# Kernel tuning notes

Hardware: AMD Instinct MI355X
Metric: run time of the kernel (lower is better)

Reference implementation:

```python
import jax, jax.numpy as jnp
import numpy as np

DIM = 1024
NUM_HEADS = 16
DIM_PER_HEAD = 64
INNER = NUM_HEADS * DIM_PER_HEAD  # 1024
SCALE = DIM_PER_HEAD ** -0.5
EPS = 1e-10


def setup_inputs() -> dict:
    key = jax.random.key(0)
    k_x, k_m, k_qkv, k_wo, k_bo = jax.random.split(key, 5)
    b, l = 2, 2048
    x = jax.random.normal(k_x, (b, l, DIM), dtype=jnp.float32)
    # binary multiplicative mask [b, l, l]
    mask = jax.random.randint(k_m, (b, l, l), 0, 2).astype(jnp.float32)
    # nn.Linear(dim, 3*inner, bias=False): weight [3*inner, dim]; we store transposed [dim, 3*inner]
    W_qkv = jax.random.normal(k_qkv, (DIM, 3 * INNER), dtype=jnp.float32) * (DIM ** -0.5)
    W_out = jax.random.normal(k_wo, (INNER, DIM), dtype=jnp.float32) * (INNER ** -0.5)
    b_out = jax.random.normal(k_bo, (DIM,), dtype=jnp.float32) * 0.01
    return {"x": x, "mask": mask, "W_qkv": W_qkv, "W_out": W_out, "b_out": b_out}


def reference(x, mask, W_qkv, W_out, b_out):
    b, l, d = x.shape
    qkv = x @ W_qkv  # [b, l, 3*inner]
    qkv = qkv.reshape(b, l, 3, NUM_HEADS, DIM_PER_HEAD)
    qkv = jnp.transpose(qkv, (2, 0, 3, 1, 4))  # [3, b, h, l, dh]
    q, k, v = qkv[0], qkv[1], qkv[2]
    # softmax FIRST (no additive mask), matching the original module
    attn = jax.nn.softmax(jnp.einsum('bhid,bhjd->bhij', q, k) * SCALE, axis=-1)  # [b,h,l,l]
    # multiplicative mask then renormalize
    attn = attn * mask[:, None, :, :]
    attn = attn / (jnp.sum(attn, axis=-1, keepdims=True) + EPS)
    z = jnp.einsum('bhij,bhjd->bhid', attn, v)  # [b,h,l,dh]
    z = jnp.transpose(z, (0, 2, 1, 3)).reshape(b, l, INNER)
    out = z @ W_out + b_out  # dropout p=0 -> identity
    return out
```

## Files before the change

### kernel.cpp

```cpp
#include <hip/hip_runtime.h>
#include <hip/hip_bf16.h>

#define BATCH 2
#define SEQ   2048
#define DIM   1024
#define HEADS 16
#define DH    64
#define N_QKV 3072
#define M_TOT 4096
#define SCALE 0.125f
#define EPS   1e-10f
#define LOG2E 1.442695041f

typedef __attribute__((ext_vector_type(8))) _Float16 half8;
typedef __attribute__((ext_vector_type(4))) float f32x4;

static __device__ __forceinline__ unsigned short f2h(float f) {
    _Float16 h = (_Float16)f;
    return __builtin_bit_cast(unsigned short, h);
}
static __device__ __forceinline__ unsigned int pkrtz(float a, float b) {
#if defined(__has_builtin) && __has_builtin(__builtin_amdgcn_cvt_pkrtz)
    return __builtin_bit_cast(unsigned int, __builtin_amdgcn_cvt_pkrtz(a, b));
#else
    return (unsigned int)f2h(a) | ((unsigned int)f2h(b) << 16);
#endif
}
static __device__ __forceinline__ void glds16(const void* g, void* l) {
    __builtin_amdgcn_global_load_lds((const __attribute__((address_space(1))) void*)g,
                                     (__attribute__((address_space(3))) void*)l,
                                     16, 0, 0);
}

__global__ __launch_bounds__(256) void prepass(const float* __restrict__ x,
                                               unsigned short* __restrict__ xh,
                                               const float* __restrict__ Wq,
                                               unsigned short* __restrict__ WqT,
                                               const float* __restrict__ Wo,
                                               unsigned short* __restrict__ WoT,
                                               const float* __restrict__ mask,
                                               unsigned short* __restrict__ mbits) {
    const int bid = blockIdx.x;
    const int t   = threadIdx.x;
    __shared__ float tile[32][33];
    __shared__ unsigned char flags[16][256];

    if (bid < 4096) {
        const int i = bid * 256 + t;
        float4 v = reinterpret_cast<const float4*>(x)[i];
        uint2 o;
        o.x = pkrtz(v.x, v.y);
        o.y = pkrtz(v.z, v.w);
        reinterpret_cast<uint2*>(xh)[i] = o;
    } else if (bid < 8192) {
        const float* src; unsigned short* th; int rows, cols, bx;
        if (bid < 7168) { src = Wq; th = WqT; rows = 1024; cols = 3072; bx = bid - 4096;
        } else          { src = Wo; th = WoT; rows = 1024; cols = 1024; bx = bid - 7168; }
        const int nbx = cols / 32;
        const int c0 = (bx % nbx) * 32, r0 = (bx / nbx) * 32;
        const int tx = t & 31, ty = t >> 5;
        #pragma unroll
        for (int i = ty; i < 32; i += 8)
            tile[i][tx] = src[(long)(r0 + i) * cols + c0 + tx];
        __syncthreads();
        #pragma unroll
        for (int i = ty; i < 32; i += 8)
            th[(long)(c0 + i) * rows + r0 + tx] = f2h(tile[tx][i]);
    } else {
        const int bx = bid - 8192;
        const int it = bx & 127;
        const int bb = bx >> 7;
        const int R0 = it * 16;
        const int tl = t >> 6, ln = t & 63;
        for (int c0 = 0; c0 < SEQ; c0 += 256) {
            #pragma unroll
            for (int rr = 0; rr < 16; ++rr)
                flags[rr][t] = mask[((long)bb * SEQ + R0 + rr) * SEQ + c0 + t] != 0.f;
            __syncthreads();
            unsigned int bits = 0;
            #pragma unroll
            for (int nt = 0; nt < 4; ++nt)
                #pragma unroll
                for (int r = 0; r < 4; ++r)
                    bits |= (unsigned int)flags[ln & 15][tl * 64 + nt * 16 + ((ln >> 4) << 2) + r]
                            << (nt * 4 + r);
            mbits[(((long)bb * 128 + it) * 32 + (c0 >> 6) + tl) * 64 + ln] = (unsigned short)bits;
            __syncthreads();
        }
    }
}

__global__ __launch_bounds__(256, 3) void gemm_qkv_f16(
    const unsigned short* __restrict__ Ahg, const unsigned short* __restrict__ Bhg,
    unsigned short* __restrict__ qb, unsigned short* __restrict__ kb,
    unsigned short* __restrict__ vtb) {
    __shared__ __align__(16) unsigned short As[128 * 64];
    __shared__ __align__(16) unsigned short Bs[128 * 64];

    const int n0   = blockIdx.x * 128;
    const int m0   = blockIdx.y * 128;
    const int wave = threadIdx.x >> 6;
    const int lane = threadIdx.x & 63;
    const int l16  = lane & 15;
    const int g    = lane >> 4;
    const int wm   = wave & 1;
    const int wn   = wave >> 1;
    const int sw   = l16 & 7;

    const int sr8 = lane >> 3;
    const int scg = (lane & 7) ^ sr8;

    f32x4 acc[4][4] = {};

    for (int k0 = 0; k0 < DIM; k0 += 64) {
        #pragma unroll
        for (int i = 0; i < 4; ++i) {
            const int row = wave * 32 + i * 8;
            glds16(Ahg + (long)(m0 + row + sr8) * DIM + k0 + scg * 8, &As[row * 64]);
            glds16(Bhg + (long)(n0 + row + sr8) * DIM + k0 + scg * 8, &Bs[row * 64]);
        }
        __syncthreads();

        #pragma unroll
        for (int kc = 0; kc < 2; ++kc) {
            half8 a[4], b[4];
            #pragma unroll
            for (int mt = 0; mt < 4; ++mt)
                a[mt] = *reinterpret_cast<const half8*>(
                    &As[(wm * 64 + mt * 16 + l16) * 64 + (((kc * 4 + g) ^ sw) * 8)]);
            #pragma unroll
            for (int nt = 0; nt < 4; ++nt)
                b[nt] = *reinterpret_cast<const half8*>(
                    &Bs[(wn * 64 + nt * 16 + l16) * 64 + (((kc * 4 + g) ^ sw) * 8)]);
            #pragma unroll
            for (int mt = 0; mt < 4; ++mt)
                #pragma unroll
                for (int nt = 0; nt < 4; ++nt)
                    acc[mt][nt] = __builtin_amdgcn_mfma_f32_16x16x32_f16(
                        a[mt], b[nt], acc[mt][nt], 0, 0, 0);
        }
        __syncthreads();
    }

    #pragma unroll
    for (int nt = 0; nt < 4; ++nt) {
        const int n     = n0 + wn * 64 + nt * 16 + l16;
        const int which = n >> 10;
        const int rem   = n & 1023;
        const int head  = rem >> 6;
        const int d     = rem & 63;
        #pragma unroll
        for (int mt = 0; mt < 4; ++mt) {
            #pragma unroll
            for (int r = 0; r < 4; ++r) {
                const int m  = m0 + wm * 64 + mt * 16 + g * 4 + r;
                const int bb = m >> 11;
                const int li = m & 2047;
                const int bh_i = bb * HEADS + head;
                const float val = acc[mt][nt][r];
                if (which == 0)
                    qb[((long)bh_i * SEQ + li) * DH + d] = f2h(val * (SCALE * LOG2E));
                else if (which == 1)
                    kb[((long)bh_i * SEQ + li) * DH + d] = f2h(val);
                else
                    vtb[((long)bh_i * DH + d) * SEQ + li] = f2h(val);
            }
        }
    }
}

__global__ __launch_bounds__(256, 4) void gemm_out_f16(
    const unsigned short* __restrict__ Ahg, const unsigned short* __restrict__ Bhg,
    const float* __restrict__ bias, float* __restrict__ out) {
    __shared__ __align__(16) unsigned short As[64 * 64];
    __shared__ __align__(16) unsigned short Bs[64 * 64];

    const int n0   = blockIdx.x * 64;
    const int m0   = blockIdx.y * 64;
    const int wave = threadIdx.x >> 6;
    const int lane = threadIdx.x & 63;
    const int l16  = lane & 15;
    const int g    = lane >> 4;
    const int wm   = wave & 1;
    const int wn   = wave >> 1;
    const int sw   = l16 & 7;

    const int sr8 = lane >> 3;
    const int scg = (lane & 7) ^ sr8;

    f32x4 acc[2][2] = {};

    for (int k0 = 0; k0 < DIM; k0 += 64) {
        #pragma unroll
        for (int i = 0; i < 2; ++i) {
            const int row = wave * 16 + i * 8;
            glds16(Ahg + (long)(m0 + row + sr8) * DIM + k0 + scg * 8, &As[row * 64]);
            glds16(Bhg + (long)(n0 + row + sr8) * DIM + k0 + scg * 8, &Bs[row * 64]);
        }
        __syncthreads();

        half8 a[2][2];
        #pragma unroll
        for (int mt = 0; mt < 2; ++mt) {
            const int rbase = (wm * 32 + mt * 16 + l16) * 64;
            #pragma unroll
            for (int kc = 0; kc < 2; ++kc)
                a[mt][kc] = *reinterpret_cast<const half8*>(
                    &As[rbase + (((kc * 4 + g) ^ sw) * 8)]);
        }
        #pragma unroll
        for (int nt = 0; nt < 2; ++nt) {
            const int rbase = (wn * 32 + nt * 16 + l16) * 64;
            const half8 b0 = *reinterpret_cast<const half8*>(&Bs[rbase + (((0 + g) ^ sw) * 8)]);
            const half8 b1 = *reinterpret_cast<const half8*>(&Bs[rbase + (((4 + g) ^ sw) * 8)]);
            #pragma unroll
            for (int mt = 0; mt < 2; ++mt) {
                acc[mt][nt] = __builtin_amdgcn_mfma_f32_16x16x32_f16(a[mt][0], b0, acc[mt][nt], 0, 0, 0);
                acc[mt][nt] = __builtin_amdgcn_mfma_f32_16x16x32_f16(a[mt][1], b1, acc[mt][nt], 0, 0, 0);
            }
        }
        __syncthreads();
    }

    #pragma unroll
    for (int nt = 0; nt < 2; ++nt) {
        const int n  = n0 + wn * 32 + nt * 16 + l16;
        const float bv = bias[n];
        #pragma unroll
        for (int mt = 0; mt < 2; ++mt) {
            #pragma unroll
            for (int r = 0; r < 4; ++r) {
                const int m = m0 + wm * 32 + mt * 16 + g * 4 + r;
                out[(long)m * DIM + n] = acc[mt][nt][r] + bv;
            }
        }
    }
}

__global__ __launch_bounds__(512, 4) void attn_mfma(const unsigned short* __restrict__ qb,
                                                    const unsigned short* __restrict__ kb,
                                                    const unsigned short* __restrict__ vtb,
                                                    const unsigned short* __restrict__ mbits,
                                                    unsigned short* __restrict__ zh) {
    const int qt   = blockIdx.x;
    const int h    = blockIdx.y;
    const int bb   = blockIdx.z;
    const int bh   = bb * HEADS + h;
    const int wave = threadIdx.x >> 6;
    const int lane = threadIdx.x & 63;
    const int l16  = lane & 15;
    const int g    = lane >> 4;
    const int wm   = wave >> 1;
    const int wj   = wave & 1;

    const int myrow0 = qt * 128 + wm * 32;

    __shared__ __align__(16) unsigned short shm[32768];

    const int sr8 = lane >> 3;
    const int scg = (lane & 7) ^ sr8;
    const int sw  = l16 & 7;

    unsigned short* Ks = &shm[wj * 8192];
    unsigned short* Vs = &shm[wj * 8192 + 4096];
    unsigned short* P0 = &shm[16384 + wave * 1024];
    unsigned short* P1 = &shm[24576 + wave * 1024];

    const unsigned short* qptr = qb + ((long)bh * SEQ + myrow0 + l16) * DH + g * 8;
    const half8 q0 = *reinterpret_cast<const half8*>(qptr);
    const half8 q1 = *reinterpret_cast<const half8*>(qptr + 32);
    const half8 q2 = *reinterpret_cast<const half8*>(qptr + 16 * DH);
    const half8 q3 = *reinterpret_cast<const half8*>(qptr + 16 * DH + 32);

    half8 ones;
    #pragma unroll
    for (int j = 0; j < 8; ++j) ones[j] = (_Float16)1.0f;

    f32x4 o0[4] = {}, o1[4] = {};
    f32x4 oz0 = {0.f, 0.f, 0.f, 0.f};
    f32x4 oz1 = {0.f, 0.f, 0.f, 0.f};

    const unsigned short* mb =
        mbits + (((long)bb * 128 + qt * 8 + wm * 2) * 32 + wj * 16) * 64 + lane;
    const long kbase = (long)bh * SEQ * DH;
    const long vbase = (long)bh * DH * SEQ;
    const int  jb    = wj * 1024;

    for (int it = 0; it < 16; ++it) {
        const int j0 = jb + it * 64;
        const unsigned int bits0 = mb[(long)it * 64];
        const unsigned int bits1 = mb[(long)it * 64 + 2048];

        #pragma unroll
        for (int i = 0; i < 2; ++i) {
            const int row = wm * 16 + i * 8;
            glds16(kb  + kbase + (long)(j0 + row + sr8) * DH + scg * 8, Ks + row * 64);
            glds16(vtb + vbase + (long)(row + sr8) * SEQ + j0 + scg * 8, Vs + row * 64);
        }
        __syncthreads();

        #pragma unroll
        for (int nt = 0; nt < 4; ++nt) {
            const int rbase = (nt * 16 + l16) * 64;
            const half8 k0 = *reinterpret_cast<const half8*>(&Ks[rbase + ((0 + g) ^ sw) * 8]);
            const half8 k1 = *reinterpret_cast<const half8*>(&Ks[rbase + (((4 + g) ^ sw) * 8)]);
            f32x4 s0 = {0.f, 0.f, 0.f, 0.f};
            f32x4 s1 = {0.f, 0.f, 0.f, 0.f};
            s0 = __builtin_amdgcn_mfma_f32_16x16x32_f16(k0, q0, s0, 0, 0, 0);
            s0 = __builtin_amdgcn_mfma_f32_16x16x32_f16(k1, q1, s0, 0, 0, 0);
            s1 = __builtin_amdgcn_mfma_f32_16x16x32_f16(k0, q2, s1, 0, 0, 0);
            s1 = __builtin_amdgcn_mfma_f32_16x16x32_f16(k1, q3, s1, 0, 0, 0);

            float pa[4], pb[4];
            #pragma unroll
            for (int r = 0; r < 4; ++r) {
                const float e0 = __builtin_amdgcn_exp2f(s0[r]);
                const float e1 = __builtin_amdgcn_exp2f(s1[r]);
                pa[r] = ((bits0 >> (nt * 4 + r)) & 1u) ? e0 : 0.f;
                pb[r] = ((bits1 >> (nt * 4 + r)) & 1u) ? e1 : 0.f;
            }
            const int poff = l16 * 64 + (((2 * nt + (g >> 1)) ^ sw) * 8) + (g & 1) * 4;
            uint2 pk0, pk1;
            pk0.x = pkrtz(pa[0], pa[1]);
            pk0.y = pkrtz(pa[2], pa[3]);
            pk1.x = pkrtz(pb[0], pb[1]);
            pk1.y = pkrtz(pb[2], pb[3]);
            *reinterpret_cast<uint2*>(&P0[poff]) = pk0;
            *reinterpret_cast<uint2*>(&P1[poff]) = pk1;
        }

        const half8 pb00 = *reinterpret_cast<const half8*>(&P0[l16 * 64 + ((0 + g) ^ sw) * 8]);
        const half8 pb01 = *reinterpret_cast<const half8*>(&P0[l16 * 64 + (((4 + g) ^ sw) * 8)]);
        const half8 pb10 = *reinterpret_cast<const half8*>(&P1[l16 * 64 + ((0 + g) ^ sw) * 8]);
        const half8 pb11 = *reinterpret_cast<const half8*>(&P1[l16 * 64 + (((4 + g) ^ sw) * 8)]);

        #pragma unroll
        for (int dt = 0; dt < 4; ++dt) {
            const int vb = (dt * 16 + l16) * 64;
            const half8 v0 = *reinterpret_cast<const half8*>(&Vs[vb + ((0 + g) ^ sw) * 8]);
            const half8 v1 = *reinterpret_cast<const half8*>(&Vs[vb + (((4 + g) ^ sw) * 8)]);
            o0[dt] = __builtin_amdgcn_mfma_f32_16x16x32_f16(v0, pb00, o0[dt], 0, 0, 0);
            o0[dt] = __builtin_amdgcn_mfma_f32_16x16x32_f16(v1, pb01, o0[dt], 0, 0, 0);
            o1[dt] = __builtin_amdgcn_mfma_f32_16x16x32_f16(v0, pb10, o1[dt], 0, 0, 0);
            o1[dt] = __builtin_amdgcn_mfma_f32_16x16x32_f16(v1, pb11, o1[dt], 0, 0, 0);
        }
        oz0 = __builtin_amdgcn_mfma_f32_16x16x32_f16(ones, pb00, oz0, 0, 0, 0);
        oz0 = __builtin_amdgcn_mfma_f32_16x16x32_f16(ones, pb01, oz0, 0, 0, 0);
        oz1 = __builtin_amdgcn_mfma_f32_16x16x32_f16(ones, pb10, oz1, 0, 0, 0);
        oz1 = __builtin_amdgcn_mfma_f32_16x16x32_f16(ones, pb11, oz1, 0, 0, 0);
        __syncthreads();
    }

    float* cmb = (float*)shm;
    const int ZOFF = 128 * 68;
    const int ci0  = wm * 32 + l16;
    const int ci1  = ci0 + 16;
    if (wj == 1) {
        #pragma unroll
        for (int dt = 0; dt < 4; ++dt) {
            *reinterpret_cast<f32x4*>(&cmb[ci0 * 68 + dt * 16 + g * 4]) = o0[dt];
            *reinterpret_cast<f32x4*>(&cmb[ci1 * 68 + dt * 16 + g * 4]) = o1[dt];
        }
        if (g == 0) {
            cmb[ZOFF + ci0] = oz0[0];
            cmb[ZOFF + ci1] = oz1[0];
        }
    }
    __syncthreads();
    if (wj == 0) {
        const float Z0   = oz0[0] + cmb[ZOFF + ci0];
        const float Z1   = oz1[0] + cmb[ZOFF + ci1];
        const float inv0 = 1.f / (Z0 + 1e-30f);
        const float inv1 = 1.f / (Z1 + 1e-30f);
        const long obase0 = ((long)bb * SEQ + myrow0 + l16) * DIM + h * DH;
        const long obase1 = obase0 + (long)16 * DIM;
        #pragma unroll
        for (int dt = 0; dt < 4; ++dt) {
            const f32x4 oc0 = *reinterpret_cast<const f32x4*>(&cmb[ci0 * 68 + dt * 16 + g * 4]);
            const f32x4 oc1 = *reinterpret_cast<const f32x4*>(&cmb[ci1 * 68 + dt * 16 + g * 4]);
            uint2 pk;
            pk.x = pkrtz((o0[dt][0] + oc0[0]) * inv0, (o0[dt][1] + oc0[1]) * inv0);
            pk.y = pkrtz((o0[dt][2] + oc0[2]) * inv0, (o0[dt][3] + oc0[3]) * inv0);
            *reinterpret_cast<uint2*>(zh + obase0 + dt * 16 + g * 4) = pk;
            pk.x = pkrtz((o1[dt][0] + oc1[0]) * inv1, (o1[dt][1] + oc1[1]) * inv1);
            pk.y = pkrtz((o1[dt][2] + oc1[2]) * inv1, (o1[dt][3] + oc1[3]) * inv1);
            *reinterpret_cast<uint2*>(zh + obase1 + dt * 16 + g * 4) = pk;
        }
    }
}

extern "C" void kernel_launch(void* const* d_in, const int* in_sizes, int n_in,
                              void* d_out, int out_size, void* d_ws, size_t ws_size,
                              hipStream_t stream) {
    const float* x     = (const float*)d_in[0];
    const float* mask  = (const float*)d_in[1];
    const float* W_qkv = (const float*)d_in[2];
    const float* W_out = (const float*)d_in[3];
    const float* b_out = (const float*)d_in[4];
    float* out = (float*)d_out;

    unsigned short* ws = (unsigned short*)d_ws;
    unsigned short* xh    = ws;
    unsigned short* WqT   = xh    + 4194304;
    unsigned short* WoT   = WqT   + 3145728;
    unsigned short* qbu   = WoT   + 1048576;
    unsigned short* kbu   = qbu   + 4194304;
    unsigned short* vtb   = kbu   + 4194304;
    unsigned short* mbits = vtb   + 4194304;
    unsigned short* zz    = xh;

    prepass<<<8448, 256, 0, stream>>>(x, xh, W_qkv, WqT, W_out, WoT, mask, mbits);

    gemm_qkv_f16<<<dim3(24, 32), 256, 0, stream>>>(xh, WqT, qbu, kbu, vtb);

    attn_mfma<<<dim3(SEQ / 128, HEADS, BATCH), 512, 0, stream>>>(qbu, kbu, vtb, mbits, zz);

    gemm_out_f16<<<dim3(16, 64), 256, 0, stream>>>(zz, WoT, b_out, out);
}
```

Baseline: 229.9 us.

## Load attention K/V straight from global, remap blocks per XCD, enlarge out-GEMM tile

The attention kernel stops staging K and V tiles through LDS with block-wide barriers. Each wave now reads its K/V fragments directly from global memory (relying on L2 reuse), uses 256 threads and 64 query rows per block, and remaps the flat block index so blocks of the same head land on the same XCD. The output GEMM tile grows from 64x64 to 128x64 for more register reuse per LDS read, at the cost of lower occupancy. The main risks are more global/L2 traffic and uncoalesced 16-byte loads in attention.

```diff
diff --git a/kernel.cpp b/kernel.cpp
--- a/kernel.cpp
+++ b/kernel.cpp
@@ -169,14 +169,14 @@
     }
 }
 
-__global__ __launch_bounds__(256, 4) void gemm_out_f16(
+__global__ __launch_bounds__(256, 2) void gemm_out_f16(
     const unsigned short* __restrict__ Ahg, const unsigned short* __restrict__ Bhg,
     const float* __restrict__ bias, float* __restrict__ out) {
-    __shared__ __align__(16) unsigned short As[64 * 64];
+    __shared__ __align__(16) unsigned short As[128 * 64];
     __shared__ __align__(16) unsigned short Bs[64 * 64];
 
     const int n0   = blockIdx.x * 64;
-    const int m0   = blockIdx.y * 64;
+    const int m0   = blockIdx.y * 128;
     const int wave = threadIdx.x >> 6;
     const int lane = threadIdx.x & 63;
     const int l16  = lane & 15;
@@ -188,36 +188,38 @@
     const int sr8 = lane >> 3;
     const int scg = (lane & 7) ^ sr8;
 
-    f32x4 acc[2][2] = {};
+    f32x4 acc[4][2] = {};
 
     for (int k0 = 0; k0 < DIM; k0 += 64) {
+        #pragma unroll
+        for (int i = 0; i < 4; ++i) {
+            const int row = wave * 32 + i * 8;
+            glds16(Ahg + (long)(m0 + row + sr8) * DIM + k0 + scg * 8, &As[row * 64]);
+        }
         #pragma unroll
         for (int i = 0; i < 2; ++i) {
             const int row = wave * 16 + i * 8;
-            glds16(Ahg + (long)(m0 + row + sr8) * DIM + k0 + scg * 8, &As[row * 64]);
             glds16(Bhg + (long)(n0 + row + sr8) * DIM + k0 + scg * 8, &Bs[row * 64]);
         }
         __syncthreads();
 
-        half8 a[2][2];
-        #pragma unroll
-        for (int mt = 0; mt < 2; ++mt) {
-            const int rbase = (wm * 32 + mt * 16 + l16) * 64;
-            #pragma unroll
-            for (int kc = 0; kc < 2; ++kc)
-                a[mt][kc] = *reinterpret_cast<const half8*>(
-                    &As[rbase + (((kc * 4 + g) ^ sw) * 8)]);
-        }
-        #pragma unroll
-        for (int nt = 0; nt < 2; ++nt) {
-            const int rbase = (wn * 32 + nt * 16 + l16) * 64;
-            const half8 b0 = *reinterpret_cast<const half8*>(&Bs[rbase + (((0 + g) ^ sw) * 8)]);
-            const half8 b1 = *reinterpret_cast<const half8*>(&Bs[rbase + (((4 + g) ^ sw) * 8)]);
-            #pragma unroll
-            for (int mt = 0; mt < 2; ++mt) {
-                acc[mt][nt] = __builtin_amdgcn_mfma_f32_16x16x32_f16(a[mt][0], b0, acc[mt][nt], 0, 0, 0);
-                acc[mt][nt] = __builtin_amdgcn_mfma_f32_16x16x32_f16(a[mt][1], b1, acc[mt][nt], 0, 0, 0);
-            }
+        #pragma unroll
+        for (int kc = 0; kc < 2; ++kc) {
+            half8 a[4], b[2];
+            #pragma unroll
+            for (int mt = 0; mt < 4; ++mt)
+                a[mt] = *reinterpret_cast<const half8*>(
+                    &As[(wm * 64 + mt * 16 + l16) * 64 + (((kc * 4 + g) ^ sw) * 8)]);
+            #pragma unroll
+            for (int nt = 0; nt < 2; ++nt)
+                b[nt] = *reinterpret_cast<const half8*>(
+                    &Bs[(wn * 32 + nt * 16 + l16) * 64 + (((kc * 4 + g) ^ sw) * 8)]);
+            #pragma unroll
+            for (int mt = 0; mt < 4; ++mt)
+                #pragma unroll
+                for (int nt = 0; nt < 2; ++nt)
+                    acc[mt][nt] = __builtin_amdgcn_mfma_f32_16x16x32_f16(
+                        a[mt], b[nt], acc[mt][nt], 0, 0, 0);
         }
         __syncthreads();
     }
@@ -227,24 +229,28 @@
         const int n  = n0 + wn * 32 + nt * 16 + l16;
         const float bv = bias[n];
         #pragma unroll
-        for (int mt = 0; mt < 2; ++mt) {
+        for (int mt = 0; mt < 4; ++mt) {
             #pragma unroll
             for (int r = 0; r < 4; ++r) {
-                const int m = m0 + wm * 32 + mt * 16 + g * 4 + r;
+                const int m = m0 + wm * 64 + mt * 16 + g * 4 + r;
                 out[(long)m * DIM + n] = acc[mt][nt][r] + bv;
             }
         }
     }
 }
 
-__global__ __launch_bounds__(512, 4) void attn_mfma(const unsigned short* __restrict__ qb,
+__global__ __launch_bounds__(256, 4) void attn_mfma(const unsigned short* __restrict__ qb,
                                                     const unsigned short* __restrict__ kb,
                                                     const unsigned short* __restrict__ vtb,
                                                     const unsigned short* __restrict__ mbits,
                                                     unsigned short* __restrict__ zh) {
-    const int qt   = blockIdx.x;
-    const int h    = blockIdx.y;
-    const int bb   = blockIdx.z;
+    const int flat = blockIdx.x;
+    const int xcd  = flat & 7;
+    const int rr   = flat >> 3;
+    const int hh   = xcd + 8 * (rr >> 5);
+    const int qt   = rr & 31;
+    const int h    = hh & 15;
+    const int bb   = hh >> 4;
     const int bh   = bb * HEADS + h;
     const int wave = threadIdx.x >> 6;
     const int lane = threadIdx.x & 63;
@@ -253,18 +259,13 @@
     const int wm   = wave >> 1;
     const int wj   = wave & 1;
 
-    const int myrow0 = qt * 128 + wm * 32;
-
-    __shared__ __align__(16) unsigned short shm[32768];
-
-    const int sr8 = lane >> 3;
-    const int scg = (lane & 7) ^ sr8;
-    const int sw  = l16 & 7;
-
-    unsigned short* Ks = &shm[wj * 8192];
-    unsigned short* Vs = &shm[wj * 8192 + 4096];
-    unsigned short* P0 = &shm[16384 + wave * 1024];
-    unsigned short* P1 = &shm[24576 + wave * 1024];
+    const int myrow0 = qt * 64 + wm * 32;
+
+    __shared__ __align__(16) unsigned short shm[9216];
+    unsigned short* P0 = &shm[wave * 1024];
+    unsigned short* P1 = &shm[4096 + wave * 1024];
+
+    const int sw = l16 & 7;
 
     const unsigned short* qptr = qb + ((long)bh * SEQ + myrow0 + l16) * DH + g * 8;
     const half8 q0 = *reinterpret_cast<const half8*>(qptr);
@@ -281,29 +282,20 @@
     f32x4 oz1 = {0.f, 0.f, 0.f, 0.f};
 
     const unsigned short* mb =
-        mbits + (((long)bb * 128 + qt * 8 + wm * 2) * 32 + wj * 16) * 64 + lane;
+        mbits + (((long)bb * 128 + qt * 4 + wm * 2) * 32 + wj * 16) * 64 + lane;
     const long kbase = (long)bh * SEQ * DH;
     const long vbase = (long)bh * DH * SEQ;
-    const int  jb    = wj * 1024;
 
     for (int it = 0; it < 16; ++it) {
-        const int j0 = jb + it * 64;
+        const int j0 = wj * 1024 + it * 64;
         const unsigned int bits0 = mb[(long)it * 64];
         const unsigned int bits1 = mb[(long)it * 64 + 2048];
 
         #pragma unroll
-        for (int i = 0; i < 2; ++i) {
-            const int row = wm * 16 + i * 8;
-            glds16(kb  + kbase + (long)(j0 + row + sr8) * DH + scg * 8, Ks + row * 64);
-            glds16(vtb + vbase + (long)(row + sr8) * SEQ + j0 + scg * 8, Vs + row * 64);
-        }
-        __syncthreads();
-
-        #pragma unroll
         for (int nt = 0; nt < 4; ++nt) {
-            const int rbase = (nt * 16 + l16) * 64;
-            const half8 k0 = *reinterpret_cast<const half8*>(&Ks[rbase + ((0 + g) ^ sw) * 8]);
-            const half8 k1 = *reinterpret_cast<const half8*>(&Ks[rbase + (((4 + g) ^ sw) * 8)]);
+            const unsigned short* kp = kb + kbase + (long)(j0 + nt * 16 + l16) * DH + g * 8;
+            const half8 k0 = *reinterpret_cast<const half8*>(kp);
+            const half8 k1 = *reinterpret_cast<const half8*>(kp + 32);
             f32x4 s0 = {0.f, 0.f, 0.f, 0.f};
             f32x4 s1 = {0.f, 0.f, 0.f, 0.f};
             s0 = __builtin_amdgcn_mfma_f32_16x16x32_f16(k0, q0, s0, 0, 0, 0);
@@ -336,9 +328,9 @@
 
         #pragma unroll
         for (int dt = 0; dt < 4; ++dt) {
-            const int vb = (dt * 16 + l16) * 64;
-            const half8 v0 = *reinterpret_cast<const half8*>(&Vs[vb + ((0 + g) ^ sw) * 8]);
-            const half8 v1 = *reinterpret_cast<const half8*>(&Vs[vb + (((4 + g) ^ sw) * 8)]);
+            const unsigned short* vp = vtb + vbase + (long)(dt * 16 + l16) * SEQ + j0 + g * 8;
+            const half8 v0 = *reinterpret_cast<const half8*>(vp);
+            const half8 v1 = *reinterpret_cast<const half8*>(vp + 32);
             o0[dt] = __builtin_amdgcn_mfma_f32_16x16x32_f16(v0, pb00, o0[dt], 0, 0, 0);
             o0[dt] = __builtin_amdgcn_mfma_f32_16x16x32_f16(v1, pb01, o0[dt], 0, 0, 0);
             o1[dt] = __builtin_amdgcn_mfma_f32_16x16x32_f16(v0, pb10, o1[dt], 0, 0, 0);
@@ -348,11 +340,12 @@
         oz0 = __builtin_amdgcn_mfma_f32_16x16x32_f16(ones, pb01, oz0, 0, 0, 0);
         oz1 = __builtin_amdgcn_mfma_f32_16x16x32_f16(ones, pb10, oz1, 0, 0, 0);
         oz1 = __builtin_amdgcn_mfma_f32_16x16x32_f16(ones, pb11, oz1, 0, 0, 0);
-        __syncthreads();
-    }
+    }
+
+    __syncthreads();
 
     float* cmb = (float*)shm;
-    const int ZOFF = 128 * 68;
+    const int ZOFF = 64 * 68;
     const int ci0  = wm * 32 + l16;
     const int ci1  = ci0 + 16;
     if (wj == 1) {
@@ -413,7 +406,7 @@
 
     gemm_qkv_f16<<<dim3(24, 32), 256, 0, stream>>>(xh, WqT, qbu, kbu, vtb);
 
-    attn_mfma<<<dim3(SEQ / 128, HEADS, BATCH), 512, 0, stream>>>(qbu, kbu, vtb, mbits, zz);
-
-    gemm_out_f16<<<dim3(16, 64), 256, 0, stream>>>(zz, WoT, b_out, out);
-}
+    attn_mfma<<<1024, 256, 0, stream>>>(qbu, kbu, vtb, mbits, zz);
+
+    gemm_out_f16<<<dim3(16, 32), 256, 0, stream>>>(zz, WoT, b_out, out);
+}
```

Measured after the change: 296.2 us. 1.29x slower.
